# Kernel optimization log

Hardware: AMD Instinct MI355X
Metric: run time of the kernel (lower is better)

The kernel has to match this reference:

```python
import jax, jax.numpy as jnp
import numpy as np

B, L, D, H = 8, 1024, 768, 12
HD = D // H
EPS = 1e-5
R_EPS = 1e-12  # numerical guard for r at coincident positions


def setup_inputs() -> dict:
    key = jax.random.key(0)
    ks = jax.random.split(key, 8)
    x = jax.random.normal(ks[0], (B, L, D), dtype=jnp.float32)
    # 32x32 patch grid coordinates, same for every batch element
    g = jnp.arange(32, dtype=jnp.float32)
    yy, xx = jnp.meshgrid(g, g, indexing='ij')
    pos = jnp.broadcast_to(jnp.stack([yy.ravel(), xx.ravel()], axis=-1), (B, L, 2))
    w_norm = jnp.ones((D,), dtype=jnp.float32)
    w_in = 0.02 * jax.random.normal(ks[1], (3 * D, D), dtype=jnp.float32)
    b_in = jnp.zeros((3 * D,), dtype=jnp.float32)
    w_out = 0.02 * jax.random.normal(ks[2], (D, D), dtype=jnp.float32)
    b_out = jnp.zeros((D,), dtype=jnp.float32)
    # bias params [H, 6] = (o, c, w, p, delta, m) per init_bias_params
    o = jnp.zeros((H,), dtype=jnp.float32)
    c = 1.0 + 0.3 * jax.random.uniform(ks[3], (H,), dtype=jnp.float32)
    w = jnp.ones((H,), dtype=jnp.float32)
    p = jnp.zeros((H,), dtype=jnp.float32)
    delta = jax.random.normal(ks[4], (H,), dtype=jnp.float32)
    m = jnp.ones((H,), dtype=jnp.float32)
    bias_params = jnp.stack([o, c, w, p, delta, m], axis=-1)
    return {"x": x, "pos": pos, "w_norm": w_norm, "w_in": w_in, "b_in": b_in,
            "w_out": w_out, "b_out": b_out, "bias_params": bias_params}


def _bias_grid(pos, bias_params):
    # pos: [B, L, 2] -> bias: [B, H, L, L]
    o, c, w, p, delta, m = [bias_params[:, i].reshape(1, H, 1, 1) for i in range(6)]
    dist = pos[:, :, None, :] - pos[:, None, :, :]          # [B, Lq, Lk, 2]
    theta = jnp.arctan2(dist[..., 1], dist[..., 0])[:, None]  # [B, 1, Lq, Lk]
    r = jnp.sqrt(jnp.sum(dist * dist, axis=-1) + R_EPS)[:, None]
    term1 = jax.nn.relu(r - o) ** jnp.abs(c)
    term2 = 1.0 - jnp.abs(jnp.tanh(delta)) * (jnp.cos((theta - p) * w * 0.5) ** 2) ** jnp.abs(m)
    return term1 * term2


def reference(x, pos, w_norm, w_in, b_in, w_out, b_out, bias_params):
    bias = _bias_grid(pos, bias_params)                      # [B, H, L, L]
    # RMSNorm
    xn = x * jax.lax.rsqrt(jnp.mean(x * x, axis=-1, keepdims=True) + EPS) * w_norm
    qkv = xn @ w_in.T + b_in                                 # [B, L, 3D]
    q, k, v = jnp.split(qkv, 3, axis=-1)
    def heads(t):
        return t.reshape(B, L, H, HD).transpose(0, 2, 1, 3)  # [B, H, L, HD]
    q, k, v = heads(q), heads(k), heads(v)
    scores = jnp.einsum('bhqd,bhkd->bhqk', q, k) / jnp.sqrt(jnp.float32(HD)) + bias
    attn = jax.nn.softmax(scores, axis=-1)
    o = jnp.einsum('bhqk,bhkd->bhqd', attn, v)
    o = o.transpose(0, 2, 1, 3).reshape(B, L, D)
    return o @ w_out.T + b_out
```

## Files before the change

kernel.cpp:

```cpp
#include <hip/hip_runtime.h>

#define BB 8
#define LL 1024
#define DD 768
#define HH 12
#define HD 64

typedef short s16x8 __attribute__((ext_vector_type(8)));
typedef float f32x4 __attribute__((ext_vector_type(4)));
typedef unsigned int u32x4 __attribute__((ext_vector_type(4)));

static __device__ __forceinline__ unsigned short f2bf(float f){
  unsigned int u = __builtin_bit_cast(unsigned int, f);
  u = (u + 0x7FFFu + ((u >> 16) & 1u)) >> 16;
  return (unsigned short)u;
}

static __device__ __forceinline__ unsigned int cvtpk_bf(float a, float b){
  unsigned int r;
  asm("v_cvt_pk_bf16_f32 %0, %1, %2" : "=v"(r) : "v"(a), "v"(b));
  return r;
}

static __device__ __forceinline__ void swap32(unsigned int& a, unsigned int& b){
  asm("v_permlane32_swap_b32 %0, %1" : "+v"(a), "+v"(b));
}
static __device__ __forceinline__ void swap16(unsigned int& a, unsigned int& b){
  asm("v_permlane16_swap_b32 %0, %1" : "+v"(a), "+v"(b));
}

static __device__ __forceinline__ float hexp2(float x){
#if __has_builtin(__builtin_amdgcn_exp2f)
  return __builtin_amdgcn_exp2f(x);
#else
  return exp2f(x);
#endif
}

static __device__ __forceinline__ f32x4 mfma16(s16x8 a, s16x8 b, f32x4 c){
  return __builtin_amdgcn_mfma_f32_16x16x32_bf16(a, b, c, 0, 0, 0);
}

static __device__ __forceinline__ void gld_lds16(const void* g, void* l){
  __builtin_amdgcn_global_load_lds(
      (const __attribute__((address_space(1))) void*)g,
      (__attribute__((address_space(3))) void*)l, 16, 0, 0);
}

__global__ __launch_bounds__(256) void prep_norm_kernel(const float* __restrict__ x,
                                                        const float* __restrict__ wn,
                                                        unsigned short* __restrict__ xn,
                                                        const float* __restrict__ w_in,
                                                        unsigned short* __restrict__ winb,
                                                        const float* __restrict__ w_out,
                                                        unsigned short* __restrict__ woutb,
                                                        const float* __restrict__ bp,
                                                        float* __restrict__ table){
  __shared__ float red[4];
  int bid = blockIdx.x, t = threadIdx.x;
  if (bid < 8192){
    int row = bid;
    const float* xr = x + (size_t)row*DD;
    float v0 = xr[t], v1 = xr[t+256], v2 = xr[t+512];
    float ss = v0*v0 + v1*v1 + v2*v2;
    #pragma unroll
    for (int m = 1; m < 64; m <<= 1) ss += __shfl_xor(ss, m, 64);
    if ((t & 63) == 0) red[t >> 6] = ss;
    __syncthreads();
    float tot = red[0] + red[1] + red[2] + red[3];
    float sc = rsqrtf(tot*(1.0f/DD) + 1e-5f);
    unsigned short* xo = xn + (size_t)row*DD;
    xo[t]     = f2bf(v0*sc*wn[t]);
    xo[t+256] = f2bf(v1*sc*wn[t+256]);
    xo[t+512] = f2bf(v2*sc*wn[t+512]);
  } else if (bid < 8192 + 1728){
    int i = (bid - 8192)*256 + t;
    float4 v = ((const float4*)w_in)[i];
    ushort4 o;
    o.x = f2bf(v.x); o.y = f2bf(v.y); o.z = f2bf(v.z); o.w = f2bf(v.w);
    ((ushort4*)winb)[i] = o;
  } else if (bid < 8192 + 2304){
    int i = (bid - 8192 - 1728)*256 + t;
    float4 v = ((const float4*)w_out)[i];
    ushort4 o;
    o.x = f2bf(v.x); o.y = f2bf(v.y); o.z = f2bf(v.z); o.w = f2bf(v.w);
    ((ushort4*)woutb)[i] = o;
  } else {
    int idx = (bid - 8192 - 2304)*256 + t;
    if (idx >= HH*3969) return;
    int hh = idx/3969, rem = idx - hh*3969;
    int dy = rem/63 - 31, dx = rem%63 - 31;
    float o  = bp[hh*6+0], c = bp[hh*6+1], w = bp[hh*6+2];
    float p  = bp[hh*6+3], dl = bp[hh*6+4], m = bp[hh*6+5];
    float theta = atan2f((float)dx, (float)dy);
    float r = sqrtf((float)(dy*dy + dx*dx) + 1e-12f);
    float t1 = powf(fmaxf(r - o, 0.0f), fabsf(c));
    float co = cosf((theta - p)*w*0.5f);
    float t2 = 1.0f - fabsf(tanhf(dl))*powf(co*co, fabsf(m));
    table[idx] = t1*t2*1.44269504f;
  }
}

__global__ __launch_bounds__(64) void bmax_kernel(const float* __restrict__ table,
                                                  float* __restrict__ bmax){
  int qy = blockIdx.x, h = blockIdx.y;
  __shared__ float m1[63];
  int t = threadIdx.x;
  const float* tb = table + h*3969;
  if (t < 63){
    float m = -3.0e38f;
    #pragma unroll 4
    for (int row = qy; row < qy + 32; row++) m = fmaxf(m, tb[row*63 + t]);
    m1[t] = m;
  }
  __syncthreads();
  if (t < 32){
    float m = -3.0e38f;
    #pragma unroll 4
    for (int c = t; c < t + 32; c++) m = fmaxf(m, m1[c]);
    bmax[(h*32 + qy)*32 + t] = m;
  }
}

template<int MODE, int TN, typename OutT>
__global__ __launch_bounds__(256) void gemm_bt_kernel(const unsigned short* __restrict__ A,
                                                      const unsigned short* __restrict__ B,
                                                      const float* __restrict__ bias,
                                                      OutT* __restrict__ C,
                                                      unsigned short* __restrict__ qp,
                                                      unsigned short* __restrict__ kp,
                                                      unsigned short* __restrict__ vt2,
                                                      int M, int N, int K){
  constexpr int NT = TN/32;
  constexpr int SMEM_BYTES = 192*(128 + TN);
  __shared__ __align__(16) char smem[SMEM_BYTES];
  unsigned short* As = (unsigned short*)smem;
  unsigned short* Bs = (unsigned short*)(smem + 3*128*32*2);
  int tid = threadIdx.x;
  int w = tid >> 6, lane = tid & 63, quad = lane >> 4, col = lane & 15;
  int wm = (w >> 1)*64, wn = (w & 1)*(TN/2);
  int bm = blockIdx.x*128, bn = blockIdx.y*TN;

  int srow = lane >> 2;
  int schunk = (((lane & 3) ^ ((lane >> 3) & 3)))*8;
  const unsigned short* ga0 = A + (size_t)(bm + w*32 + srow)*K + schunk;
  const unsigned short* ga1 = ga0 + (size_t)16*K;
  const unsigned short* gb0 = B + (size_t)(bn + w*(TN/4) + srow)*K + schunk;
  const unsigned short* gb1 = gb0 + (size_t)16*K;

  auto stage = [&](int t, int bi){
    int kk = t*32;
    gld_lds16(ga0 + kk, As + bi*4096 + (w*32)*32);
    gld_lds16(ga1 + kk, As + bi*4096 + (w*32 + 16)*32);
    gld_lds16(gb0 + kk, Bs + bi*(TN*32) + (w*(TN/4))*32);
    if (TN == 128) gld_lds16(gb1 + kk, Bs + bi*(TN*32) + (w*32 + 16)*32);
  };

  f32x4 acc[4][NT];
  #pragma unroll
  for (int mt = 0; mt < 4; mt++)
    #pragma unroll
    for (int nt = 0; nt < NT; nt++) acc[mt][nt] = (f32x4){0.f,0.f,0.f,0.f};

  stage(0, 0);
  stage(1, 1);

  int rsw = (col >> 1) & 3;
  int rchunk = (quad ^ rsw)*8;

  int KT = K >> 5;
  int buf = 0, nbuf = 2;
  for (int t = 0; t < KT; t++){
    if (t < KT - 1){
      if (TN == 128) asm volatile("s_waitcnt vmcnt(4)" ::: "memory");
      else           asm volatile("s_waitcnt vmcnt(3)" ::: "memory");
    } else {
      asm volatile("s_waitcnt vmcnt(0)" ::: "memory");
    }
    __builtin_amdgcn_s_barrier();
    asm volatile("" ::: "memory");
    if (t + 2 < KT) stage(t + 2, nbuf);
    s16x8 af[4], bfr[NT];
    #pragma unroll
    for (int mt = 0; mt < 4; mt++)
      af[mt] = *(const s16x8*)&As[buf*4096 + (wm + mt*16 + col)*32 + rchunk];
    #pragma unroll
    for (int nt = 0; nt < NT; nt++)
      bfr[nt] = *(const s16x8*)&Bs[buf*(TN*32) + (wn + nt*16 + col)*32 + rchunk];
    #pragma unroll
    for (int mt = 0; mt < 4; mt++)
      #pragma unroll
      for (int nt = 0; nt < NT; nt++)
        acc[mt][nt] = mfma16(af[mt], bfr[nt], acc[mt][nt]);
    buf  = (buf  == 2) ? 0 : buf  + 1;
    nbuf = (nbuf == 2) ? 0 : nbuf + 1;
  }

  if (MODE == 1){
    __syncthreads();
    unsigned short* Ct = (unsigned short*)smem;
    if (bn >= 1536){
      #pragma unroll
      for (int mt = 0; mt < 4; mt++)
        #pragma unroll
        for (int nt = 0; nt < NT; nt++){
          int cc = wn + nt*16 + col;
          float bv = bias[bn + cc];
          #pragma unroll
          for (int r = 0; r < 4; r++){
            int row = wm + mt*16 + quad*4 + r;
            Ct[cc*136 + row] = f2bf(acc[mt][nt][r] + bv);
          }
        }
      __syncthreads();
      int bb = bm >> 10;
      #pragma unroll
      for (int e = 0; e < 8; e++){
        int id = e*256 + tid;
        int dcol = id >> 4, rowch = id & 15;
        s16x8 val = *(const s16x8*)&Ct[dcol*136 + rowch*8];
        int cl = bn + dcol - 1536;
        int h = cl >> 6, d = cl & 63;
        int l = bm + rowch*8;
        size_t base = ((size_t)(bb*HH + h))*65536 + (size_t)((l >> 5) & 31)*2048;
        *(s16x8*)(vt2 + base + d*32 + (l & 31)) = val;
      }
    } else {
      #pragma unroll
      for (int mt = 0; mt < 4; mt++)
        #pragma unroll
        for (int nt = 0; nt < NT; nt++){
          int cc = wn + nt*16 + col;
          float bv = bias[bn + cc];
          #pragma unroll
          for (int r = 0; r < 4; r++){
            int row = wm + mt*16 + quad*4 + r;
            Ct[row*136 + cc] = f2bf(acc[mt][nt][r] + bv);
          }
        }
      __syncthreads();
      #pragma unroll
      for (int e = 0; e < 8; e++){
        int id = e*256 + tid;
        int row = id >> 4, ch = id & 15;
        s16x8 val = *(const s16x8*)&Ct[row*136 + ch*8];
        int rw = bm + row;
        int cl0 = bn + ch*8;
        int part = cl0 >= 768 ? 1 : 0;
        int hd = cl0 - part*768;
        int hh2 = hd >> 6, d0 = hd & 63;
        int bb = rw >> 10, l = rw & 1023;
        size_t base = (((size_t)bb*HH + hh2)*LL + l)*64;
        if (part == 0) *(s16x8*)(qp + base + d0) = val;
        else           *(s16x8*)(kp + base + (((d0>>3) ^ (l&7)) << 3)) = val;
      }
    }
  } else {
    __syncthreads();
    float* Cf = (float*)smem;
    #pragma unroll
    for (int mt = 0; mt < 4; mt++)
      #pragma unroll
      for (int nt = 0; nt < NT; nt++){
        int cc = wn + nt*16 + col;
        float bv = bias[bn + cc];
        #pragma unroll
        for (int r = 0; r < 4; r++){
          int row = wm + mt*16 + quad*4 + r;
          Cf[row*68 + cc] = acc[mt][nt][r] + bv;
        }
      }
    __syncthreads();
    #pragma unroll
    for (int e = 0; e < 8; e++){
      int id = e*256 + tid;
      int row = id >> 4, ch = id & 15;
      float4 val = *(const float4*)&Cf[row*68 + ch*4];
      *(float4*)&C[(size_t)(bm + row)*N + bn + ch*4] = val;
    }
  }
}

__global__ __launch_bounds__(128) void attn_kernel(const unsigned short* __restrict__ qp,
                                                   const unsigned short* __restrict__ kp,
                                                   const unsigned short* __restrict__ vt2,
                                                   const float* __restrict__ table,
                                                   const float* __restrict__ bmax,
                                                   const float* __restrict__ pos,
                                                   unsigned short* __restrict__ o_out){
  int i = blockIdx.x;
  int bh = (i >> 7)*8 + (i & 7);
  int qt = (i >> 3) & 7;
  int wp = (i >> 6) & 1;
  int b = bh/HH, h = bh - b*HH;
  int tid = threadIdx.x, w = tid >> 6, lane = tid & 63, quad = lane >> 4, col = lane & 15;
  __shared__ float tl[3969];

  const unsigned short* kgp = kp  + (size_t)bh*65536;
  const unsigned short* vgp = vt2 + (size_t)bh*65536;

  int sw = col & 7;
  int k_r0 = col*64 + ((quad ^ sw) << 3);
  int k_r1 = col*64 + (((quad + 4) ^ sw) << 3);
  int v_r  = col*32 + quad*8;

  s16x8 kA[4], vA[4], kB[4], vB[4];
  auto issue = [&](int t, s16x8 (&k)[4], s16x8 (&v)[4]){
    const unsigned short* kt = kgp + t*2048;
    const unsigned short* vt = vgp + t*2048;
    k[0] = *(const s16x8*)(kt + k_r0);
    k[1] = *(const s16x8*)(kt + k_r1);
    k[2] = *(const s16x8*)(kt + 1024 + k_r0);
    k[3] = *(const s16x8*)(kt + 1024 + k_r1);
    v[0] = *(const s16x8*)(vt + v_r);
    v[1] = *(const s16x8*)(vt + v_r + 512);
    v[2] = *(const s16x8*)(vt + v_r + 1024);
    v[3] = *(const s16x8*)(vt + v_r + 1536);
  };
  issue(0, kA, vA);
  issue(1, kB, vB);

  for (int j = tid; j < 3969; j += 128) tl[j] = table[h*3969 + j];
  const float* pb = pos + (size_t)b*2048;

  int qw = qt*128 + (wp*2 + w)*32;
  const unsigned short* qpb = qp + (size_t)bh*65536;
  s16x8 qa[2][2];
  int cq[2];
  f32x4 zb[2];
  #pragma unroll
  for (int g = 0; g < 2; g++){
    int q = qw + g*16 + col;
    size_t qo = (size_t)q*64 + quad*8;
    qa[g][0] = *(const s16x8*)(qpb + qo);
    qa[g][1] = *(const s16x8*)(qpb + qo + 32);
    int qy = __float2int_rn(pb[q*2]);
    int qx = __float2int_rn(pb[q*2 + 1]);
    cq[g] = qy*63 + qx + 1984 - quad*4;
    float neg = -5.5451774445f * bmax[(h*32 + qy)*32 + qx];
    zb[g] = (f32x4){neg, neg, neg, neg};
  }

  s16x8 ones;
  #pragma unroll
  for (int e = 0; e < 8; e++) ones[e] = (short)0x3F80;

  f32x4 o[2][4];
  f32x4 l_acc[2];
  #pragma unroll
  for (int g = 0; g < 2; g++){
    #pragma unroll
    for (int nt = 0; nt < 4; nt++) o[g][nt] = (f32x4){0.f,0.f,0.f,0.f};
    l_acc[g] = (f32x4){0.f,0.f,0.f,0.f};
  }

  __syncthreads();

  auto step = [&](int t, s16x8 (&k)[4], s16x8 (&v)[4]){
    int kyt = 63*t;
    #pragma unroll
    for (int g = 0; g < 2; g++){
      f32x4 s_lo = mfma16(k[0], qa[g][0], zb[g]);  s_lo = mfma16(k[1], qa[g][1], s_lo);
      f32x4 s_hi = mfma16(k[2], qa[g][0], zb[g]);  s_hi = mfma16(k[3], qa[g][1], s_hi);
      int base = cq[g] - kyt;
      float pl[4], ph[4];
      #pragma unroll
      for (int r = 0; r < 4; r++){
        pl[r] = hexp2(__builtin_fmaf(s_lo[r], 0.18033688f, tl[base - r]));
        ph[r] = hexp2(__builtin_fmaf(s_hi[r], 0.18033688f, tl[base - r - 16]));
      }
      unsigned int wA = cvtpk_bf(pl[0], pl[1]);
      unsigned int wB = cvtpk_bf(pl[2], pl[3]);
      unsigned int wC = cvtpk_bf(ph[0], ph[1]);
      unsigned int wD = cvtpk_bf(ph[2], ph[3]);
      swap32(wA, wC);  swap32(wB, wD);
      swap16(wA, wC);  swap16(wB, wD);
      u32x4 pv4; pv4.x = wA; pv4.y = wB; pv4.z = wC; pv4.w = wD;
      s16x8 pf = __builtin_bit_cast(s16x8, pv4);
      l_acc[g] = mfma16(ones, pf, l_acc[g]);
      o[g][0] = mfma16(v[0], pf, o[g][0]);
      o[g][1] = mfma16(v[1], pf, o[g][1]);
      o[g][2] = mfma16(v[2], pf, o[g][2]);
      o[g][3] = mfma16(v[3], pf, o[g][3]);
    }
  };

  for (int t = 0; t < 32; t += 2){
    step(t, kA, vA);
    if (t + 2 < 32) issue(t + 2, kA, vA);
    step(t + 1, kB, vB);
    if (t + 3 < 32) issue(t + 3, kB, vB);
  }

  #pragma unroll
  for (int g = 0; g < 2; g++){
    float inv = 1.0f / l_acc[g][0];
    int q = qw + g*16 + col;
    unsigned short* orow = o_out + (size_t)(b*LL + q)*DD + h*64;
    #pragma unroll
    for (int nt = 0; nt < 4; nt++){
      uint2 pkd;
      pkd.x = cvtpk_bf(o[g][nt][0]*inv, o[g][nt][1]*inv);
      pkd.y = cvtpk_bf(o[g][nt][2]*inv, o[g][nt][3]*inv);
      *(uint2*)&orow[nt*16 + quad*4] = pkd;
    }
  }
}

extern "C" void kernel_launch(void* const* d_in, const int* in_sizes, int n_in,
                              void* d_out, int out_size, void* d_ws, size_t ws_size,
                              hipStream_t stream){
  const float* x      = (const float*)d_in[0];
  const float* pos    = (const float*)d_in[1];
  const float* w_norm = (const float*)d_in[2];
  const float* w_in   = (const float*)d_in[3];
  const float* b_in   = (const float*)d_in[4];
  const float* w_out  = (const float*)d_in[5];
  const float* b_out  = (const float*)d_in[6];
  const float* bp     = (const float*)d_in[7];

  char* ws = (char*)d_ws;
  unsigned short* xn    = (unsigned short*)(ws);
  unsigned short* winb  = (unsigned short*)(ws + 12582912);
  unsigned short* woutb = (unsigned short*)(ws + 16121856);
  unsigned short* qpb   = (unsigned short*)(ws + 17301504);
  unsigned short* kpb   = (unsigned short*)(ws + 29884416);
  unsigned short* vt2b  = (unsigned short*)(ws + 55050240);
  float*          table = (float*)        (ws + 67633152);
  unsigned short* ob    = (unsigned short*)(ws + 67823664);
  float*          bmaxp = (float*)        (ws);

  prep_norm_kernel<<<dim3(8192 + 2491), dim3(256), 0, stream>>>(
      x, w_norm, xn, w_in, winb, w_out, woutb, bp, table);
  gemm_bt_kernel<1, 128, unsigned short><<<dim3(64, 18), dim3(256), 0, stream>>>(
      xn, winb, b_in, (unsigned short*)nullptr, qpb, kpb, vt2b, BB*LL, 3*DD, DD);
  bmax_kernel<<<dim3(32, HH), dim3(64), 0, stream>>>(table, bmaxp);
  attn_kernel<<<dim3(1536), dim3(128), 0, stream>>>(qpb, kpb, vt2b, table, bmaxp, pos, ob);
  gemm_bt_kernel<0, 64, float><<<dim3(64, 12), dim3(256), 0, stream>>>(
      ob, woutb, b_out, (float*)d_out, nullptr, nullptr, nullptr, BB*LL, DD, DD);
}
```

Baseline: 218.3 us.

## Fold bmax into QKV GEMM launch and widen attention blocks to four waves

The separate bmax kernel is removed. Its work now runs as 384 extra blocks appended to a flattened 1D grid of the QKV projection GEMM, so one launch and its dependency gap disappear. The bmax buffer moves to a workspace region that no longer aliases xn, because the two now run concurrently. The attention kernel goes from 128 to 256 threads per block with half as many blocks, so each per-head bias table copy into LDS is shared by four waves instead of two. The risks are extra LDS and register pressure per block, which could lower occupancy in attention, and tail imbalance from the small bmax blocks mixed into the GEMM grid.

```diff
diff --git a/kernel.cpp b/kernel.cpp
--- a/kernel.cpp
+++ b/kernel.cpp
@@ -101,27 +101,6 @@
   }
 }
 
-__global__ __launch_bounds__(64) void bmax_kernel(const float* __restrict__ table,
-                                                  float* __restrict__ bmax){
-  int qy = blockIdx.x, h = blockIdx.y;
-  __shared__ float m1[63];
-  int t = threadIdx.x;
-  const float* tb = table + h*3969;
-  if (t < 63){
-    float m = -3.0e38f;
-    #pragma unroll 4
-    for (int row = qy; row < qy + 32; row++) m = fmaxf(m, tb[row*63 + t]);
-    m1[t] = m;
-  }
-  __syncthreads();
-  if (t < 32){
-    float m = -3.0e38f;
-    #pragma unroll 4
-    for (int c = t; c < t + 32; c++) m = fmaxf(m, m1[c]);
-    bmax[(h*32 + qy)*32 + t] = m;
-  }
-}
-
 template<int MODE, int TN, typename OutT>
 __global__ __launch_bounds__(256) void gemm_bt_kernel(const unsigned short* __restrict__ A,
                                                       const unsigned short* __restrict__ B,
@@ -130,16 +109,43 @@
                                                       unsigned short* __restrict__ qp,
                                                       unsigned short* __restrict__ kp,
                                                       unsigned short* __restrict__ vt2,
+                                                      const float* __restrict__ tablep,
+                                                      float* __restrict__ bmx,
                                                       int M, int N, int K){
   constexpr int NT = TN/32;
   constexpr int SMEM_BYTES = 192*(128 + TN);
   __shared__ __align__(16) char smem[SMEM_BYTES];
+  int tid = threadIdx.x;
+
+  if (MODE == 1 && (int)blockIdx.x >= 1152){
+    float* m1 = (float*)smem;
+    int idx = blockIdx.x - 1152;
+    int qy = idx & 31, h = idx >> 5;
+    const float* tb = tablep + h*3969;
+    if (tid < 63){
+      float m = -3.0e38f;
+      #pragma unroll 4
+      for (int row = qy; row < qy + 32; row++) m = fmaxf(m, tb[row*63 + tid]);
+      m1[tid] = m;
+    }
+    __syncthreads();
+    if (tid < 32){
+      float m = -3.0e38f;
+      #pragma unroll 4
+      for (int c = tid; c < tid + 32; c++) m = fmaxf(m, m1[c]);
+      bmx[(h*32 + qy)*32 + tid] = m;
+    }
+    return;
+  }
+
   unsigned short* As = (unsigned short*)smem;
   unsigned short* Bs = (unsigned short*)(smem + 3*128*32*2);
-  int tid = threadIdx.x;
   int w = tid >> 6, lane = tid & 63, quad = lane >> 4, col = lane & 15;
   int wm = (w >> 1)*64, wn = (w & 1)*(TN/2);
-  int bm = blockIdx.x*128, bn = blockIdx.y*TN;
+  int bx, by;
+  if (MODE == 1){ bx = blockIdx.x & 63; by = blockIdx.x >> 6; }
+  else          { bx = blockIdx.x;      by = blockIdx.y; }
+  int bm = bx*128, bn = by*TN;
 
   int srow = lane >> 2;
   int schunk = (((lane & 3) ^ ((lane >> 3) & 3)))*8;
@@ -281,7 +287,7 @@
   }
 }
 
-__global__ __launch_bounds__(128) void attn_kernel(const unsigned short* __restrict__ qp,
+__global__ __launch_bounds__(256) void attn_kernel(const unsigned short* __restrict__ qp,
                                                    const unsigned short* __restrict__ kp,
                                                    const unsigned short* __restrict__ vt2,
                                                    const float* __restrict__ table,
@@ -289,9 +295,8 @@
                                                    const float* __restrict__ pos,
                                                    unsigned short* __restrict__ o_out){
   int i = blockIdx.x;
-  int bh = (i >> 7)*8 + (i & 7);
+  int bh = (i >> 6)*8 + (i & 7);
   int qt = (i >> 3) & 7;
-  int wp = (i >> 6) & 1;
   int b = bh/HH, h = bh - b*HH;
   int tid = threadIdx.x, w = tid >> 6, lane = tid & 63, quad = lane >> 4, col = lane & 15;
   __shared__ float tl[3969];
@@ -320,10 +325,10 @@
   issue(0, kA, vA);
   issue(1, kB, vB);
 
-  for (int j = tid; j < 3969; j += 128) tl[j] = table[h*3969 + j];
+  for (int j = tid; j < 3969; j += 256) tl[j] = table[h*3969 + j];
   const float* pb = pos + (size_t)b*2048;
 
-  int qw = qt*128 + (wp*2 + w)*32;
+  int qw = qt*128 + w*32;
   const unsigned short* qpb = qp + (size_t)bh*65536;
   s16x8 qa[2][2];
   int cq[2];
@@ -425,17 +430,18 @@
   unsigned short* woutb = (unsigned short*)(ws + 16121856);
   unsigned short* qpb   = (unsigned short*)(ws + 17301504);
   unsigned short* kpb   = (unsigned short*)(ws + 29884416);
+  float*          bmaxp = (float*)        (ws + 42467328);
   unsigned short* vt2b  = (unsigned short*)(ws + 55050240);
   float*          table = (float*)        (ws + 67633152);
   unsigned short* ob    = (unsigned short*)(ws + 67823664);
-  float*          bmaxp = (float*)        (ws);
 
   prep_norm_kernel<<<dim3(8192 + 2491), dim3(256), 0, stream>>>(
       x, w_norm, xn, w_in, winb, w_out, woutb, bp, table);
-  gemm_bt_kernel<1, 128, unsigned short><<<dim3(64, 18), dim3(256), 0, stream>>>(
-      xn, winb, b_in, (unsigned short*)nullptr, qpb, kpb, vt2b, BB*LL, 3*DD, DD);
-  bmax_kernel<<<dim3(32, HH), dim3(64), 0, stream>>>(table, bmaxp);
-  attn_kernel<<<dim3(1536), dim3(128), 0, stream>>>(qpb, kpb, vt2b, table, bmaxp, pos, ob);
+  gemm_bt_kernel<1, 128, unsigned short><<<dim3(1536), dim3(256), 0, stream>>>(
+      xn, winb, b_in, (unsigned short*)nullptr, qpb, kpb, vt2b, table, bmaxp,
+      BB*LL, 3*DD, DD);
+  attn_kernel<<<dim3(768), dim3(256), 0, stream>>>(qpb, kpb, vt2b, table, bmaxp, pos, ob);
   gemm_bt_kernel<0, 64, float><<<dim3(64, 12), dim3(256), 0, stream>>>(
-      ob, woutb, b_out, (float*)d_out, nullptr, nullptr, nullptr, BB*LL, DD, DD);
-}
+      ob, woutb, b_out, (float*)d_out, nullptr, nullptr, nullptr, nullptr, nullptr,
+      BB*LL, DD, DD);
+}
```

After: 211.0 us. -3.3%, faster.
